# Kernel optimization log

Measured on AMD Instinct MI355X. Metric: run time of the kernel, lower is better.

## Reference

```python
import jax, jax.numpy as jnp
import numpy as np

B, L, D, H, DK, DV = 16, 1024, 512, 8, 64, 64
FACTOR = 1
TOP_K = int(FACTOR * np.log(L))  # 6, static


def autocorrelation(q, k, v, top_k):
    # q, k, v: [B, L, H, E] (Autoformer layout)
    Bs, Ls, Hs, Es = q.shape
    qp = jnp.transpose(q, (0, 2, 3, 1))  # [B,H,E,L]
    kp = jnp.transpose(k, (0, 2, 3, 1))
    vp = jnp.transpose(v, (0, 2, 3, 1))
    qf = jnp.fft.rfft(qp, axis=-1)
    kf = jnp.fft.rfft(kp, axis=-1)
    corr = jnp.fft.irfft(qf * jnp.conj(kf), n=Ls, axis=-1)  # [B,H,E,L]
    # time_delay_agg_training: average corr over heads and channels
    mean_value = corr.mean(axis=(1, 2))  # [B,L]
    _, index = jax.lax.top_k(mean_value.mean(axis=0), top_k)  # [top_k] shared delays
    weights = jnp.take(mean_value, index, axis=1)  # [B,top_k]
    tmp_corr = jax.nn.softmax(weights, axis=-1)  # [B,top_k]
    # roll(v, -delay) gathered for all top_k delays at once
    idx = (index[:, None] + jnp.arange(Ls)[None, :]) % Ls  # [top_k, L]
    patterns = vp[..., idx]  # [B,H,E,top_k,L]
    agg = jnp.einsum('bhekl,bk->bhel', patterns, tmp_corr)  # [B,H,E,L]
    return jnp.transpose(agg, (0, 3, 1, 2))  # [B,L,H,E]


def setup_inputs() -> dict:
    key = jax.random.key(0)
    ks = jax.random.split(key, 7)
    Q = jax.random.normal(ks[0], (B, L, D), jnp.float32)
    K = jax.random.normal(ks[1], (B, L, D), jnp.float32)
    V = jax.random.normal(ks[2], (B, L, D), jnp.float32)
    attn_mask = jnp.zeros((B, 1, L, L), jnp.bool_)  # ignored by AutoCorrelation
    s = 0.02
    WQ = jax.random.normal(ks[3], (D, H * DK), jnp.float32) * s
    WK = jax.random.normal(ks[4], (D, H * DK), jnp.float32) * s
    WV = jax.random.normal(ks[5], (D, H * DV), jnp.float32) * s
    Wfc = jax.random.normal(ks[6], (H * DV, D), jnp.float32) * s
    return {"Q": Q, "K": K, "V": V, "attn_mask": attn_mask,
            "WQ": WQ, "WK": WK, "WV": WV, "Wfc": Wfc}


def reference(Q, K, V, attn_mask, WQ, WK, WV, Wfc):
    del attn_mask  # full AutoCorrelation ignores the mask
    q_s = (Q @ WQ).reshape(B, L, H, DK)  # [B,L,H,dk]
    k_s = (K @ WK).reshape(B, L, H, DK)
    v_s = (V @ WV).reshape(B, L, H, DV)
    out = autocorrelation(q_s, k_s, v_s, TOP_K)  # [B,L,H,dv]
    context = out.reshape(B, L, H * DV)
    return context @ Wfc  # [B,L,D]
```

## Files before the change

kernel.cpp:

```cpp
#include <hip/hip_runtime.h>
#include <math.h>

namespace {

constexpr int Bb = 16;
constexpr int Ll = 1024;
constexpr int Dd = 512;
constexpr int TOPK = 6;
constexpr int Kc = 512;

typedef short  short8 __attribute__((ext_vector_type(8)));
typedef float  f32x4  __attribute__((ext_vector_type(4)));

__device__ __forceinline__ short f2bf(float x) {
  unsigned u = __builtin_bit_cast(unsigned, x);
  u += 0x7fffu + ((u >> 16) & 1u);
  return (short)(u >> 16);
}
__device__ __forceinline__ float bf2f(short b) {
  unsigned u = ((unsigned)(unsigned short)b) << 16;
  return __builtin_bit_cast(float, u);
}
__device__ __forceinline__ void g2l16(const void* g, void* l) {
  __builtin_amdgcn_global_load_lds(
      (const __attribute__((address_space(1))) unsigned*)g,
      (__attribute__((address_space(3))) unsigned*)l, 16, 0, 0);
}
__device__ __forceinline__ short8 cvt8(float4 a, float4 b) {
  short8 o;
  o[0] = f2bf(a.x); o[1] = f2bf(a.y); o[2] = f2bf(a.z); o[3] = f2bf(a.w);
  o[4] = f2bf(b.x); o[5] = f2bf(b.y); o[6] = f2bf(b.z); o[7] = f2bf(b.w);
  return o;
}

#define BARRIER() do { asm volatile("" ::: "memory"); \
    __builtin_amdgcn_s_barrier(); \
    asm volatile("" ::: "memory"); } while (0)
#define VMCNT8() asm volatile("s_waitcnt vmcnt(8)" ::: "memory")
#define VMCNT4() asm volatile("s_waitcnt vmcnt(4)" ::: "memory")
#define VMCNT0() asm volatile("s_waitcnt vmcnt(0)" ::: "memory")
#define LGKM0()  do { asm volatile("s_waitcnt lgkmcnt(0)" ::: "memory"); \
    __builtin_amdgcn_sched_barrier(0); } while (0)

template<int MODE>
__global__ __launch_bounds__(256) void g64(
    const void* __restrict__ A0, const void* __restrict__ A1,
    const short* __restrict__ B0, const short* __restrict__ B1,
    void* __restrict__ C0, void* __restrict__ C1)
{
  __shared__ short lds[2][16384];
  __shared__ float bins[256];

  const int tid = threadIdx.x;
  int z, m0, n0;
  if (MODE == 0) {
    z = blockIdx.x >> 4;
    const int s = blockIdx.x & 15;
    m0 = (s >> 2) * 128;  n0 = (s & 3) * 128;
  } else if (MODE == 1) {
    z = blockIdx.z;
    const int fb = blockIdx.x;
    const int s  = (fb & 7) * 64 + (fb >> 3);
    m0 = (s >> 2) * 128;  n0 = (s & 3) * 128;
  } else {
    const int fb = blockIdx.x;
    const int s  = (fb & 7) * 128 + (fb >> 3);
    z  = s >> 6;
    m0 = ((s >> 3) & 7) * 128;  n0 = (s & 7) * 128;
  }

  const int rS  = tid >> 3;
  const int c8S = (tid & 7) ^ (rS & 7);
  const short* Ga = nullptr;  const float* Fa = nullptr;
  const short* Gb = nullptr;  const float* Fb = nullptr;
  if (MODE == 0) {
    Ga = (const short*)(z ? A1 : A0) + (size_t)(m0 + rS) * Kc + c8S * 8;
    Gb = (z ? B1 : B0) + (size_t)(n0 + rS) * Kc + c8S * 8;
  } else if (MODE == 1) {
    Fa = (const float*)(z ? A1 : A0) + (size_t)(m0 + rS) * Kc + c8S * 8;
    Gb = (z ? B1 : B0) + (size_t)(n0 + rS) * Kc + c8S * 8;
  } else {
    Ga = (const short*)A0 + (size_t)z * Ll * Kc + (size_t)(m0 + rS) * Kc + c8S * 8;
    Fb = (const float*)A1 + (size_t)z * Ll * Kc + (size_t)(n0 + rS) * Kc + c8S * 8;
  }

  const int lane = tid & 63;
  const int wid  = tid >> 6;
  const int wr = wid >> 1, wn = wid & 1;
  const int lo = lane & 15, hi = lane >> 4;
  int aoff[2][4], boff[2][4];
#pragma unroll
  for (int i = 0; i < 4; ++i) {
    const int ar = wr * 64 + i * 16 + lo;
    const int br = wn * 64 + i * 16 + lo;
#pragma unroll
    for (int ks = 0; ks < 2; ++ks) {
      aoff[ks][i] = (ar * 8 + ((ks * 4 + hi) ^ (ar & 7))) * 8;
      boff[ks][i] = 8192 + (br * 8 + ((ks * 4 + hi) ^ (br & 7))) * 8;
    }
  }

  if (MODE == 2) bins[tid] = 0.f;

  f32x4 acc[4][4];
#pragma unroll
  for (int i = 0; i < 4; ++i)
#pragma unroll
    for (int j = 0; j < 4; ++j) acc[i][j] = (f32x4){0.f, 0.f, 0.f, 0.f};

#define SG_A(buf, kt) do { _Pragma("unroll") \
    for (int i_ = 0; i_ < 4; ++i_) \
      g2l16(Ga + (size_t)i_ * 32 * Kc + (kt) * 64, &lds[buf][(i_ * 256 + tid) * 8]); } while (0)
#define SG_B(buf, kt) do { _Pragma("unroll") \
    for (int i_ = 0; i_ < 4; ++i_) \
      g2l16(Gb + (size_t)i_ * 32 * Kc + (kt) * 64, &lds[buf][8192 + (i_ * 256 + tid) * 8]); } while (0)
#define LD_F(eV, F, kt) do { _Pragma("unroll") \
    for (int i_ = 0; i_ < 4; ++i_) { \
      eV[2 * i_]     = *(const float4*)((F) + (size_t)i_ * 32 * Kc + (kt) * 64); \
      eV[2 * i_ + 1] = *(const float4*)((F) + (size_t)i_ * 32 * Kc + (kt) * 64 + 4); } } while (0)
#define WR_F(buf, opb, eV) do { _Pragma("unroll") \
    for (int i_ = 0; i_ < 4; ++i_) \
      *(short8*)&lds[buf][(opb) + (i_ * 256 + tid) * 8] = cvt8(eV[2 * i_], eV[2 * i_ + 1]); } while (0)

  {
    float4 e[8];
    if (MODE == 1) {
      SG_B(0, 0); LD_F(e, Fa, 0); WR_F(0, 0, e);
      SG_B(1, 1); LD_F(e, Fa, 1); WR_F(1, 0, e);
    } else if (MODE == 2) {
      SG_A(0, 0); LD_F(e, Fb, 0); WR_F(0, 8192, e);
      SG_A(1, 1); LD_F(e, Fb, 1); WR_F(1, 8192, e);
    } else {
      SG_A(0, 0); SG_B(0, 0);
      SG_A(1, 1); SG_B(1, 1);
    }
  }

  int cur = 0;
#pragma unroll 1
  for (int t = 0; t < 8; ++t) {
    if (t == 7)            VMCNT0();
    else if (MODE == 0)    VMCNT8();
    else                   VMCNT4();
    LGKM0();
    BARRIER();

    const short* L = lds[cur];
    const bool pf = (t < 6);
    float4 e[8];

    short8 af[4], bq[4];
#pragma unroll
    for (int i = 0; i < 4; ++i) af[i] = *(const short8*)(L + aoff[0][i]);
#pragma unroll
    for (int j = 0; j < 4; ++j) bq[j] = *(const short8*)(L + boff[0][j]);
    if (pf && MODE == 1) LD_F(e, Fa, t + 2);
    if (pf && MODE == 2) LD_F(e, Fb, t + 2);
#pragma unroll
    for (int i = 0; i < 4; ++i)
#pragma unroll
      for (int j = 0; j < 4; ++j)
        acc[i][j] = __builtin_amdgcn_mfma_f32_16x16x32_bf16(af[i], bq[j], acc[i][j], 0, 0, 0);
#pragma unroll
    for (int i = 0; i < 4; ++i) af[i] = *(const short8*)(L + aoff[1][i]);
#pragma unroll
    for (int j = 0; j < 4; ++j) bq[j] = *(const short8*)(L + boff[1][j]);
#pragma unroll
    for (int i = 0; i < 4; ++i)
#pragma unroll
      for (int j = 0; j < 4; ++j)
        acc[i][j] = __builtin_amdgcn_mfma_f32_16x16x32_bf16(af[i], bq[j], acc[i][j], 0, 0, 0);

    BARRIER();

    if (pf) {
      if (MODE == 1)      { SG_B(cur, t + 2); WR_F(cur, 0, e); }
      else if (MODE == 2) { SG_A(cur, t + 2); WR_F(cur, 8192, e); }
      else                { SG_A(cur, t + 2); SG_B(cur, t + 2); }
    }
    cur ^= 1;
  }
#undef SG_A
#undef SG_B
#undef LD_F
#undef WR_F

  if (MODE != 2) {
    short* C = (short*)(MODE == 0 ? (z ? C1 : C0) : (z ? C1 : C0));
#pragma unroll
    for (int i = 0; i < 4; ++i)
#pragma unroll
      for (int r = 0; r < 4; ++r) {
        const size_t row = m0 + wr * 64 + i * 16 + hi * 4 + r;
#pragma unroll
        for (int j = 0; j < 4; ++j)
          C[row * Dd + n0 + wn * 64 + j * 16 + lo] = f2bf(acc[i][j][r]);
      }
  } else {
    float red[7][4];
#pragma unroll
    for (int d = 0; d < 7; ++d)
#pragma unroll
      for (int r = 0; r < 4; ++r) red[d][r] = 0.f;
#pragma unroll
    for (int i = 0; i < 4; ++i)
#pragma unroll
      for (int j = 0; j < 4; ++j)
#pragma unroll
        for (int r = 0; r < 4; ++r) red[i - j + 3][r] += acc[i][j][r];

    const int dbase = 127 + (wr - wn) * 64 + 4 * hi - lo;
#pragma unroll
    for (int d = 0; d < 7; ++d)
#pragma unroll
      for (int r = 0; r < 4; ++r)
        atomicAdd(&bins[dbase + 16 * (d - 3) + r], red[d][r]);
    __syncthreads();
    if (tid < 255) {
      float* mv = (float*)C0;
      const int l = (m0 - n0 + tid - 127) & (Ll - 1);
      atomicAdd(&mv[z * Ll + l], bins[tid]);
    }
  }
}

__global__ __launch_bounds__(256) void prep(
    const float* __restrict__ WQ, const float* __restrict__ WK,
    const float* __restrict__ WV, const float* __restrict__ Wfc,
    short* __restrict__ wqb, short* __restrict__ wkb,
    short* __restrict__ wvb, short* __restrict__ wtf,
    float* __restrict__ mv)
{
  const int z = blockIdx.z;
  const int tx = threadIdx.x & 31, ty = threadIdx.x >> 5;
  const int bx = blockIdx.x, by = blockIdx.y;
  if (z < 3) {
    const float* W = (z == 0) ? WQ : (z == 1) ? WK : WV;
    short* O = (z == 0) ? wqb : (z == 1) ? wkb : wvb;
#pragma unroll
    for (int s = 0; s < 32; s += 8) {
      const size_t o = (size_t)(by * 32 + ty + s) * 512 + bx * 32 + tx;
      O[o] = f2bf(W[o]);
    }
    if (z == 0 && threadIdx.x < 64) {
      const int fb = by * 16 + bx;
      mv[fb * 64 + threadIdx.x] = 0.f;
    }
  } else {
    __shared__ float t[32][33];
#pragma unroll
    for (int s = 0; s < 32; s += 8)
      t[ty + s][tx] = Wfc[(size_t)(by * 32 + ty + s) * 512 + bx * 32 + tx];
    __syncthreads();
#pragma unroll
    for (int s = 0; s < 32; s += 8)
      wtf[(size_t)(bx * 32 + ty + s) * 512 + by * 32 + tx] = f2bf(t[tx][ty + s]);
  }
}

__global__ __launch_bounds__(1024) void topk_softmax(
    const float* __restrict__ mean_value,
    int* __restrict__ idx_out, float* __restrict__ w_out)
{
  __shared__ float vals[1024];
  __shared__ int   inds[1024];
  __shared__ float bm[1024];
  __shared__ int   topi[TOPK];
  const int t = threadIdx.x;
  float s = 0.f;
  for (int b = 0; b < Bb; ++b) s += mean_value[b * Ll + t];
  bm[t] = s;
  __syncthreads();
  for (int k = 0; k < TOPK; ++k) {
    bool taken = false;
    for (int j = 0; j < k; ++j) taken |= (topi[j] == t);
    vals[t] = taken ? -INFINITY : bm[t];
    inds[t] = t;
    __syncthreads();
    for (int stride = 512; stride > 0; stride >>= 1) {
      if (t < stride) {
        if (vals[t + stride] > vals[t]) { vals[t] = vals[t + stride]; inds[t] = inds[t + stride]; }
      }
      __syncthreads();
    }
    if (t == 0) topi[k] = inds[0];
    __syncthreads();
  }
  if (t < TOPK) idx_out[t] = topi[t];
  if (t < Bb) {
    float wv[TOPK], mx = -INFINITY;
#pragma unroll
    for (int k = 0; k < TOPK; ++k) {
      wv[k] = mean_value[t * Ll + topi[k]] * (1.f / 512.f);
      mx = fmaxf(mx, wv[k]);
    }
    float sum = 0.f;
#pragma unroll
    for (int k = 0; k < TOPK; ++k) { wv[k] = expf(wv[k] - mx); sum += wv[k]; }
#pragma unroll
    for (int k = 0; k < TOPK; ++k) w_out[t * TOPK + k] = wv[k] / sum;
  }
}

__global__ __launch_bounds__(256) void gather_out(
    const short* __restrict__ U, const float* __restrict__ w,
    const int* __restrict__ idx, float* __restrict__ out)
{
  const int b = blockIdx.y;
  __shared__ float ww[8];
  __shared__ int   ii[8];
  if (threadIdx.x < TOPK) { ww[threadIdx.x] = w[b * TOPK + threadIdx.x]; ii[threadIdx.x] = idx[threadIdx.x]; }
  __syncthreads();
  const int l = blockIdx.x * 4 + (threadIdx.x >> 6);
  const int c = (threadIdx.x & 63) * 8;
  const short* ub = U + (size_t)b * Ll * Dd;
  float a[8] = {};
#pragma unroll
  for (int k = 0; k < TOPK; ++k) {
    const short8 vv = *(const short8*)&ub[(size_t)((l + ii[k]) & (Ll - 1)) * Dd + c];
    const float wk = ww[k];
#pragma unroll
    for (int e = 0; e < 8; ++e) a[e] = fmaf(wk, bf2f(vv[e]), a[e]);
  }
  float* op = &out[((size_t)b * Ll + l) * Dd + c];
  *(float4*)op       = make_float4(a[0], a[1], a[2], a[3]);
  *(float4*)(op + 4) = make_float4(a[4], a[5], a[6], a[7]);
}

}

extern "C" void kernel_launch(void* const* d_in, const int* in_sizes, int n_in,
                              void* d_out, int out_size, void* d_ws, size_t ws_size,
                              hipStream_t stream)
{
  const float* Q   = (const float*)d_in[0];
  const float* K   = (const float*)d_in[1];
  const float* V   = (const float*)d_in[2];
  const float* WQ  = (const float*)d_in[4];
  const float* WK  = (const float*)d_in[5];
  const float* WV  = (const float*)d_in[6];
  const float* Wfc = (const float*)d_in[7];
  float* out = (float*)d_out;

  char* ws = (char*)d_ws;
  const size_t SB = (size_t)Bb * Ll * Dd * sizeof(short);
  short* T    = (short*)(ws);
  short* U    = (short*)(ws + 1 * SB);
  short* wqb  = (short*)(ws + 2 * SB);
  short* wkb  = wqb + 512 * 512;
  short* wvb  = wkb + 512 * 512;
  short* wtf  = wvb + 512 * 512;
  short* Gt   = wtf + 512 * 512;
  short* Ht   = Gt  + 512 * 512;
  float* mv   = (float*)(Ht + 512 * 512);
  float* w    = mv + Bb * Ll;
  int*   idx  = (int*)(w + 128);

  prep<<<dim3(16, 16, 4), 256, 0, stream>>>(WQ, WK, WV, Wfc, wqb, wkb, wvb, wtf, mv);

  g64<0><<<32, 256, 0, stream>>>(wkb, wtf, wqb, wvb, Gt, Ht);

  g64<1><<<dim3(512, 1, 2), 256, 0, stream>>>(Q, V, Gt, Ht, T, U);

  g64<2><<<1024, 256, 0, stream>>>(T, K, nullptr, nullptr, mv, nullptr);

  topk_softmax<<<1, 1024, 0, stream>>>(mv, idx, w);

  gather_out<<<dim3(Ll / 4, Bb), 256, 0, stream>>>(U, w, idx, out);
}
```

Before: 138.4 us.

## Move correlation GEMM to dedicated 256x256-tile kernel with 1024 threads

Splits the MODE 2 correlation-diagonal GEMM out of the shared g64 template into a new corr_gemm kernel. It uses 256x256 output tiles, 16 waves per block and 32-wide K steps with a double-buffered LDS pipeline. The diagonal-bin reduction now covers 511 delay bins per block, which halves the global atomics per output area and raises operand reuse. In exchange there are four times fewer blocks (256), a barrier on every K step, and higher register and LDS pressure per block that may reduce latency hiding.

```diff
diff --git a/kernel.cpp b/kernel.cpp
--- a/kernel.cpp
+++ b/kernel.cpp
@@ -49,7 +49,6 @@
     void* __restrict__ C0, void* __restrict__ C1)
 {
   __shared__ short lds[2][16384];
-  __shared__ float bins[256];
 
   const int tid = threadIdx.x;
   int z, m0, n0;
@@ -57,31 +56,23 @@
     z = blockIdx.x >> 4;
     const int s = blockIdx.x & 15;
     m0 = (s >> 2) * 128;  n0 = (s & 3) * 128;
-  } else if (MODE == 1) {
+  } else {
     z = blockIdx.z;
     const int fb = blockIdx.x;
     const int s  = (fb & 7) * 64 + (fb >> 3);
     m0 = (s >> 2) * 128;  n0 = (s & 3) * 128;
-  } else {
-    const int fb = blockIdx.x;
-    const int s  = (fb & 7) * 128 + (fb >> 3);
-    z  = s >> 6;
-    m0 = ((s >> 3) & 7) * 128;  n0 = (s & 7) * 128;
   }
 
   const int rS  = tid >> 3;
   const int c8S = (tid & 7) ^ (rS & 7);
   const short* Ga = nullptr;  const float* Fa = nullptr;
-  const short* Gb = nullptr;  const float* Fb = nullptr;
+  const short* Gb = nullptr;
   if (MODE == 0) {
     Ga = (const short*)(z ? A1 : A0) + (size_t)(m0 + rS) * Kc + c8S * 8;
     Gb = (z ? B1 : B0) + (size_t)(n0 + rS) * Kc + c8S * 8;
-  } else if (MODE == 1) {
+  } else {
     Fa = (const float*)(z ? A1 : A0) + (size_t)(m0 + rS) * Kc + c8S * 8;
     Gb = (z ? B1 : B0) + (size_t)(n0 + rS) * Kc + c8S * 8;
-  } else {
-    Ga = (const short*)A0 + (size_t)z * Ll * Kc + (size_t)(m0 + rS) * Kc + c8S * 8;
-    Fb = (const float*)A1 + (size_t)z * Ll * Kc + (size_t)(n0 + rS) * Kc + c8S * 8;
   }
 
   const int lane = tid & 63;
@@ -99,8 +90,6 @@
       boff[ks][i] = 8192 + (br * 8 + ((ks * 4 + hi) ^ (br & 7))) * 8;
     }
   }
-
-  if (MODE == 2) bins[tid] = 0.f;
 
   f32x4 acc[4][4];
 #pragma unroll
@@ -127,9 +116,6 @@
     if (MODE == 1) {
       SG_B(0, 0); LD_F(e, Fa, 0); WR_F(0, 0, e);
       SG_B(1, 1); LD_F(e, Fa, 1); WR_F(1, 0, e);
-    } else if (MODE == 2) {
-      SG_A(0, 0); LD_F(e, Fb, 0); WR_F(0, 8192, e);
-      SG_A(1, 1); LD_F(e, Fb, 1); WR_F(1, 8192, e);
     } else {
       SG_A(0, 0); SG_B(0, 0);
       SG_A(1, 1); SG_B(1, 1);
@@ -155,7 +141,6 @@
 #pragma unroll
     for (int j = 0; j < 4; ++j) bq[j] = *(const short8*)(L + boff[0][j]);
     if (pf && MODE == 1) LD_F(e, Fa, t + 2);
-    if (pf && MODE == 2) LD_F(e, Fb, t + 2);
 #pragma unroll
     for (int i = 0; i < 4; ++i)
 #pragma unroll
@@ -175,7 +160,6 @@
 
     if (pf) {
       if (MODE == 1)      { SG_B(cur, t + 2); WR_F(cur, 0, e); }
-      else if (MODE == 2) { SG_A(cur, t + 2); WR_F(cur, 8192, e); }
       else                { SG_A(cur, t + 2); SG_B(cur, t + 2); }
     }
     cur ^= 1;
@@ -185,42 +169,123 @@
 #undef LD_F
 #undef WR_F
 
-  if (MODE != 2) {
-    short* C = (short*)(MODE == 0 ? (z ? C1 : C0) : (z ? C1 : C0));
+  short* C = (short*)(z ? C1 : C0);
+#pragma unroll
+  for (int i = 0; i < 4; ++i)
+#pragma unroll
+    for (int r = 0; r < 4; ++r) {
+      const size_t row = m0 + wr * 64 + i * 16 + hi * 4 + r;
+#pragma unroll
+      for (int j = 0; j < 4; ++j)
+        C[row * Dd + n0 + wn * 64 + j * 16 + lo] = f2bf(acc[i][j][r]);
+    }
+}
+
+__global__ __launch_bounds__(1024) void corr_gemm(
+    const short* __restrict__ T, const float* __restrict__ Kf,
+    float* __restrict__ mv)
+{
+  __shared__ short lds[2][16384];
+  __shared__ float bins[512];
+
+  const int tid = threadIdx.x;
+  const int fb = blockIdx.x;
+  const int s  = (fb & 7) * 32 + (fb >> 3);
+  const int z  = s >> 4;
+  const int m0 = ((s >> 2) & 3) * 256;
+  const int n0 = (s & 3) * 256;
+
+  const short* Ab = T  + (size_t)z * Ll * Dd;
+  const float* Bf = Kf + (size_t)z * Ll * Dd;
+
+  const int rS  = tid >> 2;
+  const int c8S = (tid & 3) ^ ((rS >> 1) & 3);
+  const short* gA = Ab + (size_t)(m0 + rS) * Dd + c8S * 8;
+  const float* gB = Bf + (size_t)(n0 + rS) * Dd + c8S * 8;
+  const int dB = 8192 + tid * 8;
+
+  const int lane = tid & 63;
+  const int wid  = tid >> 6;
+  const int wm = wid >> 2, wn = wid & 3;
+  const int lo = lane & 15, hi = lane >> 4;
+  int aoff[4], boff[4];
+#pragma unroll
+  for (int i = 0; i < 4; ++i) {
+    const int ar = wm * 64 + i * 16 + lo;
+    aoff[i] = (ar * 4 + (hi ^ ((ar >> 1) & 3))) * 8;
+  }
+#pragma unroll
+  for (int j = 0; j < 4; ++j) {
+    const int br = wn * 64 + j * 16 + lo;
+    boff[j] = 8192 + (br * 4 + (hi ^ ((br >> 1) & 3))) * 8;
+  }
+
+  if (tid < 512) bins[tid] = 0.f;
+
+  f32x4 acc[4][4];
+#pragma unroll
+  for (int i = 0; i < 4; ++i)
+#pragma unroll
+    for (int j = 0; j < 4; ++j) acc[i][j] = (f32x4){0.f, 0.f, 0.f, 0.f};
+
+  {
+    g2l16(gA, &lds[0][tid * 8]);
+    const float4 a = *(const float4*)(gB);
+    const float4 b = *(const float4*)(gB + 4);
+    *(short8*)&lds[0][dB] = cvt8(a, b);
+  }
+  __syncthreads();
+
+#pragma unroll 1
+  for (int t = 0; t < 16; ++t) {
+    const int cur = t & 1;
+    const short* L = &lds[cur][0];
+    short8 af[4], bfr[4];
+#pragma unroll
+    for (int i = 0; i < 4; ++i) af[i]  = *(const short8*)(L + aoff[i]);
+#pragma unroll
+    for (int j = 0; j < 4; ++j) bfr[j] = *(const short8*)(L + boff[j]);
+
+    float4 e0, e1;
+    if (t < 15) {
+      const int ke = (t + 1) * 32;
+      g2l16(gA + ke, &lds[cur ^ 1][tid * 8]);
+      e0 = *(const float4*)(gB + ke);
+      e1 = *(const float4*)(gB + ke + 4);
+    }
+
 #pragma unroll
     for (int i = 0; i < 4; ++i)
 #pragma unroll
-      for (int r = 0; r < 4; ++r) {
-        const size_t row = m0 + wr * 64 + i * 16 + hi * 4 + r;
-#pragma unroll
-        for (int j = 0; j < 4; ++j)
-          C[row * Dd + n0 + wn * 64 + j * 16 + lo] = f2bf(acc[i][j][r]);
-      }
-  } else {
-    float red[7][4];
-#pragma unroll
-    for (int d = 0; d < 7; ++d)
-#pragma unroll
-      for (int r = 0; r < 4; ++r) red[d][r] = 0.f;
-#pragma unroll
-    for (int i = 0; i < 4; ++i)
-#pragma unroll
       for (int j = 0; j < 4; ++j)
-#pragma unroll
-        for (int r = 0; r < 4; ++r) red[i - j + 3][r] += acc[i][j][r];
-
-    const int dbase = 127 + (wr - wn) * 64 + 4 * hi - lo;
-#pragma unroll
-    for (int d = 0; d < 7; ++d)
-#pragma unroll
-      for (int r = 0; r < 4; ++r)
-        atomicAdd(&bins[dbase + 16 * (d - 3) + r], red[d][r]);
+        acc[i][j] = __builtin_amdgcn_mfma_f32_16x16x32_bf16(af[i], bfr[j], acc[i][j], 0, 0, 0);
+
+    if (t < 15) *(short8*)&lds[cur ^ 1][dB] = cvt8(e0, e1);
     __syncthreads();
-    if (tid < 255) {
-      float* mv = (float*)C0;
-      const int l = (m0 - n0 + tid - 127) & (Ll - 1);
-      atomicAdd(&mv[z * Ll + l], bins[tid]);
-    }
+  }
+
+  float red[7][4];
+#pragma unroll
+  for (int d = 0; d < 7; ++d)
+#pragma unroll
+    for (int r = 0; r < 4; ++r) red[d][r] = 0.f;
+#pragma unroll
+  for (int i = 0; i < 4; ++i)
+#pragma unroll
+    for (int j = 0; j < 4; ++j)
+#pragma unroll
+      for (int r = 0; r < 4; ++r) red[i - j + 3][r] += acc[i][j][r];
+
+  const int dbase = 255 + (wm - wn) * 64 + 4 * hi - lo;
+#pragma unroll
+  for (int d = 0; d < 7; ++d)
+#pragma unroll
+    for (int r = 0; r < 4; ++r)
+      atomicAdd(&bins[dbase + 16 * (d - 3) + r], red[d][r]);
+  __syncthreads();
+  if (tid < 511) {
+    const int l = (m0 - n0 + tid - 255) & (Ll - 1);
+    atomicAdd(&mv[z * Ll + l], bins[tid]);
   }
 }
 
@@ -362,7 +427,7 @@
 
   g64<1><<<dim3(512, 1, 2), 256, 0, stream>>>(Q, V, Gt, Ht, T, U);
 
-  g64<2><<<1024, 256, 0, stream>>>(T, K, nullptr, nullptr, mv, nullptr);
+  corr_gemm<<<256, 1024, 0, stream>>>(T, K, mv);
 
   topk_softmax<<<1, 1024, 0, stream>>>(mv, idx, w);
 
```

Result: faster. 132.1 us (-4.5%).

## Replace dense lag-correlation GEMM with per-channel FFT cross-spectrum and inverse FFT

Applied to the files above, without the earlier changes.

The old MODE 2 path got the mean autocorrelation through a 1024x1024 GEMM per batch (T·Kᵀ) with diagonal binning. The new path writes T transposed per channel, transposes K to bf16 in spare blocks of the first GEMM launch, then runs a packed complex FFT of q and k per channel. It accumulates the conjugate cross-spectrum over 16 channels per block and atomically sums into a per-batch spectrum, and a small kernel takes the inverse FFT to produce mean_value. This cuts the O(L²) correlation work to O(L log L), at the cost of LDS-bound butterflies with a barrier per stage, extra transpose traffic, and float atomics.

```diff
diff --git a/kernel.cpp b/kernel.cpp
--- a/kernel.cpp
+++ b/kernel.cpp
@@ -9,6 +9,7 @@
 constexpr int TOPK = 6;
 constexpr int Kc = 512;
 
+typedef short  short4v __attribute__((ext_vector_type(4)));
 typedef short  short8 __attribute__((ext_vector_type(8)));
 typedef float  f32x4  __attribute__((ext_vector_type(4)));
 
@@ -31,6 +32,9 @@
   o[0] = f2bf(a.x); o[1] = f2bf(a.y); o[2] = f2bf(a.z); o[3] = f2bf(a.w);
   o[4] = f2bf(b.x); o[5] = f2bf(b.y); o[6] = f2bf(b.z); o[7] = f2bf(b.w);
   return o;
+}
+__device__ __forceinline__ int rev10(int k) {
+  return (int)(__builtin_bitreverse32((unsigned)k) >> 22);
 }
 
 #define BARRIER() do { asm volatile("" ::: "memory"); \
@@ -46,42 +50,58 @@
 __global__ __launch_bounds__(256) void g64(
     const void* __restrict__ A0, const void* __restrict__ A1,
     const short* __restrict__ B0, const short* __restrict__ B1,
-    void* __restrict__ C0, void* __restrict__ C1)
+    void* __restrict__ C0, void* __restrict__ C1,
+    const float* __restrict__ KfIn, short* __restrict__ kbOut)
 {
   __shared__ short lds[2][16384];
-  __shared__ float bins[256];
 
   const int tid = threadIdx.x;
   int z, m0, n0;
   if (MODE == 0) {
+    if (blockIdx.x >= 32) {
+      float (*tf)[33] = (float(*)[33])lds;
+      const int ci = blockIdx.x - 32;
+      const int r8 = tid >> 5, cc = tid & 31;
+      const int her = tid >> 3, c4 = (tid & 7) * 4;
+#pragma unroll 1
+      for (int it = 0; it < 16; ++it) {
+        const int tile = ci * 16 + it;
+        const int b  = tile >> 9;
+        const int ti = (tile >> 4) & 31;
+        const int hh = tile & 15;
+        const float* src = KfIn + ((size_t)b * 1024 + ti * 32) * 512 + hh * 32;
+#pragma unroll
+        for (int rr = 0; rr < 4; ++rr)
+          tf[r8 + rr * 8][cc] = src[(size_t)(r8 + rr * 8) * 512 + cc];
+        __syncthreads();
+        short4v o;
+#pragma unroll
+        for (int e = 0; e < 4; ++e) o[e] = f2bf(tf[c4 + e][her]);
+        *(short4v*)&kbOut[((size_t)b * 512 + hh * 32 + her) * 1024 + ti * 32 + c4] = o;
+        __syncthreads();
+      }
+      return;
+    }
     z = blockIdx.x >> 4;
     const int s = blockIdx.x & 15;
     m0 = (s >> 2) * 128;  n0 = (s & 3) * 128;
-  } else if (MODE == 1) {
+  } else {
     z = blockIdx.z;
     const int fb = blockIdx.x;
     const int s  = (fb & 7) * 64 + (fb >> 3);
     m0 = (s >> 2) * 128;  n0 = (s & 3) * 128;
-  } else {
-    const int fb = blockIdx.x;
-    const int s  = (fb & 7) * 128 + (fb >> 3);
-    z  = s >> 6;
-    m0 = ((s >> 3) & 7) * 128;  n0 = (s & 7) * 128;
   }
 
   const int rS  = tid >> 3;
   const int c8S = (tid & 7) ^ (rS & 7);
   const short* Ga = nullptr;  const float* Fa = nullptr;
-  const short* Gb = nullptr;  const float* Fb = nullptr;
+  const short* Gb = nullptr;
   if (MODE == 0) {
     Ga = (const short*)(z ? A1 : A0) + (size_t)(m0 + rS) * Kc + c8S * 8;
     Gb = (z ? B1 : B0) + (size_t)(n0 + rS) * Kc + c8S * 8;
-  } else if (MODE == 1) {
+  } else {
     Fa = (const float*)(z ? A1 : A0) + (size_t)(m0 + rS) * Kc + c8S * 8;
     Gb = (z ? B1 : B0) + (size_t)(n0 + rS) * Kc + c8S * 8;
-  } else {
-    Ga = (const short*)A0 + (size_t)z * Ll * Kc + (size_t)(m0 + rS) * Kc + c8S * 8;
-    Fb = (const float*)A1 + (size_t)z * Ll * Kc + (size_t)(n0 + rS) * Kc + c8S * 8;
   }
 
   const int lane = tid & 63;
@@ -99,8 +119,6 @@
       boff[ks][i] = 8192 + (br * 8 + ((ks * 4 + hi) ^ (br & 7))) * 8;
     }
   }
-
-  if (MODE == 2) bins[tid] = 0.f;
 
   f32x4 acc[4][4];
 #pragma unroll
@@ -127,9 +145,6 @@
     if (MODE == 1) {
       SG_B(0, 0); LD_F(e, Fa, 0); WR_F(0, 0, e);
       SG_B(1, 1); LD_F(e, Fa, 1); WR_F(1, 0, e);
-    } else if (MODE == 2) {
-      SG_A(0, 0); LD_F(e, Fb, 0); WR_F(0, 8192, e);
-      SG_A(1, 1); LD_F(e, Fb, 1); WR_F(1, 8192, e);
     } else {
       SG_A(0, 0); SG_B(0, 0);
       SG_A(1, 1); SG_B(1, 1);
@@ -155,7 +170,6 @@
 #pragma unroll
     for (int j = 0; j < 4; ++j) bq[j] = *(const short8*)(L + boff[0][j]);
     if (pf && MODE == 1) LD_F(e, Fa, t + 2);
-    if (pf && MODE == 2) LD_F(e, Fb, t + 2);
 #pragma unroll
     for (int i = 0; i < 4; ++i)
 #pragma unroll
@@ -175,7 +189,6 @@
 
     if (pf) {
       if (MODE == 1)      { SG_B(cur, t + 2); WR_F(cur, 0, e); }
-      else if (MODE == 2) { SG_A(cur, t + 2); WR_F(cur, 8192, e); }
       else                { SG_A(cur, t + 2); SG_B(cur, t + 2); }
     }
     cur ^= 1;
@@ -185,8 +198,23 @@
 #undef LD_F
 #undef WR_F
 
-  if (MODE != 2) {
-    short* C = (short*)(MODE == 0 ? (z ? C1 : C0) : (z ? C1 : C0));
+  if (MODE == 1 && z == 0) {
+    short* Tt = (short*)C0;
+#pragma unroll
+    for (int i = 0; i < 4; ++i) {
+      const int rowb = m0 + wr * 64 + i * 16 + hi * 4;
+      const size_t bbase = (size_t)(rowb >> 10) * 512;
+#pragma unroll
+      for (int j = 0; j < 4; ++j) {
+        const int col = n0 + wn * 64 + j * 16 + lo;
+        short4v o;
+#pragma unroll
+        for (int r = 0; r < 4; ++r) o[r] = f2bf(acc[i][j][r]);
+        *(short4v*)&Tt[(bbase + col) * 1024 + (rowb & 1023)] = o;
+      }
+    }
+  } else {
+    short* C = (short*)(z ? C1 : C0);
 #pragma unroll
     for (int i = 0; i < 4; ++i)
 #pragma unroll
@@ -196,32 +224,124 @@
         for (int j = 0; j < 4; ++j)
           C[row * Dd + n0 + wn * 64 + j * 16 + lo] = f2bf(acc[i][j][r]);
       }
-  } else {
-    float red[7][4];
-#pragma unroll
-    for (int d = 0; d < 7; ++d)
-#pragma unroll
-      for (int r = 0; r < 4; ++r) red[d][r] = 0.f;
-#pragma unroll
-    for (int i = 0; i < 4; ++i)
-#pragma unroll
-      for (int j = 0; j < 4; ++j)
-#pragma unroll
-        for (int r = 0; r < 4; ++r) red[i - j + 3][r] += acc[i][j][r];
-
-    const int dbase = 127 + (wr - wn) * 64 + 4 * hi - lo;
-#pragma unroll
-    for (int d = 0; d < 7; ++d)
-#pragma unroll
-      for (int r = 0; r < 4; ++r)
-        atomicAdd(&bins[dbase + 16 * (d - 3) + r], red[d][r]);
-    __syncthreads();
-    if (tid < 255) {
-      float* mv = (float*)C0;
-      const int l = (m0 - n0 + tid - 127) & (Ll - 1);
-      atomicAdd(&mv[z * Ll + l], bins[tid]);
-    }
-  }
+  }
+}
+
+__global__ __launch_bounds__(256) void fftcorr(
+    const short* __restrict__ Tt, const short* __restrict__ kbT,
+    float* __restrict__ Sg)
+{
+  __shared__ float2 x[1024];
+  __shared__ float2 tw[512];
+  __shared__ float2 sac[513];
+
+  const int tid = threadIdx.x;
+  const int b   = blockIdx.x >> 5;
+  const int he0 = (blockIdx.x & 31) * 16;
+
+  for (int j = tid; j < 512; j += 256) {
+    float sv, cv;
+    sincosf(6.283185307179586f * (float)j / 1024.f, &sv, &cv);
+    tw[j] = make_float2(cv, -sv);
+  }
+  for (int k = tid; k < 513; k += 256) sac[k] = make_float2(0.f, 0.f);
+  __syncthreads();
+
+#pragma unroll 1
+  for (int he = 0; he < 16; ++he) {
+    const short* q = Tt  + ((size_t)b * 512 + he0 + he) * 1024;
+    const short* p = kbT + ((size_t)b * 512 + he0 + he) * 1024;
+    {
+      const int t4 = tid * 4;
+      const short4v qv = *(const short4v*)&q[t4];
+      const short4v pv = *(const short4v*)&p[t4];
+#pragma unroll
+      for (int e = 0; e < 4; ++e)
+        x[t4 + e] = make_float2(bf2f(qv[e]), bf2f(pv[e]));
+    }
+    __syncthreads();
+
+#pragma unroll
+    for (int sh = 9; sh >= 0; --sh) {
+      const int h = 1 << sh;
+#pragma unroll
+      for (int bb = 0; bb < 2; ++bb) {
+        const int bf = tid + bb * 256;
+        const int pos = bf & (h - 1);
+        const int i0 = ((bf >> sh) << (sh + 1)) + pos;
+        const int i1 = i0 + h;
+        const float2 u = x[i0], v = x[i1];
+        const float2 w = tw[pos << (9 - sh)];
+        const float2 d = make_float2(u.x - v.x, u.y - v.y);
+        x[i0] = make_float2(u.x + v.x, u.y + v.y);
+        x[i1] = make_float2(d.x * w.x - d.y * w.y, d.x * w.y + d.y * w.x);
+      }
+      __syncthreads();
+    }
+
+#pragma unroll
+    for (int kk = 0; kk < 3; ++kk) {
+      const int k = (kk < 2) ? (tid + kk * 256) : 512;
+      if (kk < 2 || tid == 0) {
+        const float2 Zk = x[rev10(k)];
+        const float2 Zm = x[rev10((1024 - k) & 1023)];
+        const float2 A = make_float2(0.5f * (Zk.x + Zm.x), 0.5f * (Zk.y - Zm.y));
+        const float2 B = make_float2(0.5f * (Zk.y + Zm.y), -0.5f * (Zk.x - Zm.x));
+        sac[k].x += A.x * B.x + A.y * B.y;
+        sac[k].y += A.y * B.x - A.x * B.y;
+      }
+    }
+    __syncthreads();
+  }
+
+  for (int k = tid; k < 513; k += 256) {
+    atomicAdd(&Sg[((size_t)b * 513 + k) * 2 + 0], sac[k].x);
+    atomicAdd(&Sg[((size_t)b * 513 + k) * 2 + 1], sac[k].y);
+  }
+}
+
+__global__ __launch_bounds__(256) void ifft_mv(
+    const float* __restrict__ Sg, float* __restrict__ mv)
+{
+  __shared__ float2 x[1024];
+  __shared__ float2 tw[512];
+  const int tid = threadIdx.x;
+  const int b = blockIdx.x;
+
+  for (int j = tid; j < 512; j += 256) {
+    float sv, cv;
+    sincosf(6.283185307179586f * (float)j / 1024.f, &sv, &cv);
+    tw[j] = make_float2(cv, sv);
+  }
+  for (int k = tid; k < 1024; k += 256) {
+    if (k <= 512)
+      x[k] = make_float2(Sg[((size_t)b * 513 + k) * 2], Sg[((size_t)b * 513 + k) * 2 + 1]);
+    else
+      x[k] = make_float2(Sg[((size_t)b * 513 + 1024 - k) * 2],
+                        -Sg[((size_t)b * 513 + 1024 - k) * 2 + 1]);
+  }
+  __syncthreads();
+
+#pragma unroll
+  for (int sh = 9; sh >= 0; --sh) {
+    const int h = 1 << sh;
+#pragma unroll
+    for (int bb = 0; bb < 2; ++bb) {
+      const int bf = tid + bb * 256;
+      const int pos = bf & (h - 1);
+      const int i0 = ((bf >> sh) << (sh + 1)) + pos;
+      const int i1 = i0 + h;
+      const float2 u = x[i0], v = x[i1];
+      const float2 w = tw[pos << (9 - sh)];
+      const float2 d = make_float2(u.x - v.x, u.y - v.y);
+      x[i0] = make_float2(u.x + v.x, u.y + v.y);
+      x[i1] = make_float2(d.x * w.x - d.y * w.y, d.x * w.y + d.y * w.x);
+    }
+    __syncthreads();
+  }
+
+  for (int l = tid; l < 1024; l += 256)
+    mv[b * 1024 + l] = x[rev10(l)].x * (1.f / 1024.f);
 }
 
 __global__ __launch_bounds__(256) void prep(
@@ -229,7 +349,7 @@
     const float* __restrict__ WV, const float* __restrict__ Wfc,
     short* __restrict__ wqb, short* __restrict__ wkb,
     short* __restrict__ wvb, short* __restrict__ wtf,
-    float* __restrict__ mv)
+    float* __restrict__ Sg)
 {
   const int z = blockIdx.z;
   const int tx = threadIdx.x & 31, ty = threadIdx.x >> 5;
@@ -242,9 +362,9 @@
       const size_t o = (size_t)(by * 32 + ty + s) * 512 + bx * 32 + tx;
       O[o] = f2bf(W[o]);
     }
-    if (z == 0 && threadIdx.x < 64) {
-      const int fb = by * 16 + bx;
-      mv[fb * 64 + threadIdx.x] = 0.f;
+    if (z == 0) {
+      const int gi = (by * 16 + bx) * 256 + (int)threadIdx.x;
+      if (gi < 16 * 513 * 2) Sg[gi] = 0.f;
     }
   } else {
     __shared__ float t[32][33];
@@ -344,9 +464,10 @@
 
   char* ws = (char*)d_ws;
   const size_t SB = (size_t)Bb * Ll * Dd * sizeof(short);
-  short* T    = (short*)(ws);
+  short* Tt   = (short*)(ws);
   short* U    = (short*)(ws + 1 * SB);
-  short* wqb  = (short*)(ws + 2 * SB);
+  short* kbT  = (short*)(ws + 2 * SB);
+  short* wqb  = (short*)(ws + 3 * SB);
   short* wkb  = wqb + 512 * 512;
   short* wvb  = wkb + 512 * 512;
   short* wtf  = wvb + 512 * 512;
@@ -355,14 +476,17 @@
   float* mv   = (float*)(Ht + 512 * 512);
   float* w    = mv + Bb * Ll;
   int*   idx  = (int*)(w + 128);
-
-  prep<<<dim3(16, 16, 4), 256, 0, stream>>>(WQ, WK, WV, Wfc, wqb, wkb, wvb, wtf, mv);
-
-  g64<0><<<32, 256, 0, stream>>>(wkb, wtf, wqb, wvb, Gt, Ht);
-
-  g64<1><<<dim3(512, 1, 2), 256, 0, stream>>>(Q, V, Gt, Ht, T, U);
-
-  g64<2><<<1024, 256, 0, stream>>>(T, K, nullptr, nullptr, mv, nullptr);
+  float* Sg   = (float*)(idx + 64);
+
+  prep<<<dim3(16, 16, 4), 256, 0, stream>>>(WQ, WK, WV, Wfc, wqb, wkb, wvb, wtf, Sg);
+
+  g64<0><<<544, 256, 0, stream>>>(wkb, wtf, wqb, wvb, Gt, Ht, K, kbT);
+
+  g64<1><<<dim3(512, 1, 2), 256, 0, stream>>>(Q, V, Gt, Ht, Tt, U, nullptr, nullptr);
+
+  fftcorr<<<512, 256, 0, stream>>>(Tt, kbT, Sg);
+
+  ifft_mv<<<16, 256, 0, stream>>>(Sg, mv);
 
   topk_softmax<<<1, 1024, 0, stream>>>(mv, idx, w);
 
```

New measurement: 159.7 us. +15.4%, slower.
